# Performance work log

Hardware: AMD Instinct MI355X
Metric: run time of the kernel (lower is better)

## Reference

```python
import jax, jax.numpy as jnp
import numpy as np

B, L, D = 8, 2048, 256
NEG = 10000.0


def setup_inputs() -> dict:
    key = jax.random.key(0)
    kq, kk, kv, km = jax.random.split(key, 4)
    return {
        "query": jax.random.normal(kq, (B, L, D), dtype=jnp.float32),
        "key": jax.random.normal(kk, (B, L, D), dtype=jnp.float32),
        "value": jax.random.normal(kv, (B, L, D), dtype=jnp.float32),
        "mask": jax.random.randint(km, (B, L), 0, 2).astype(bool),
    }


def reference(query, key, value, mask):
    d = query.shape[-1]
    # scores: [B, Lq, Lk]
    e = jnp.einsum("bqd,bkd->bqk", query, key) / jnp.sqrt(jnp.asarray(d, query.dtype))
    # history_only (causal) mask: subtract 10000 where key index > query index
    q_len, k_len = query.shape[1], key.shape[1]
    causal = (jnp.arange(k_len)[None, :] > jnp.arange(q_len)[:, None]).astype(query.dtype)
    e = e - NEG * causal[None, :, :]
    # key padding mask: [B, 1, Lk]
    e = e - NEG * (1.0 - mask.astype(query.dtype))[:, None, :]
    attn = jax.nn.softmax(e, axis=-1)
    return jnp.einsum("bqk,bkd->bqd", attn, value)
```

## Files before the change

### kernel.cpp

```cpp
#include <hip/hip_runtime.h>
#include <stdint.h>

#define NL 2048
#define ND 256
#define KVB 32
#define QB 64
#define NQT 32
#define NT_ALL (NL / KVB)
#define CHUNK 10
#define NCHUNKS_B 125
#define TILE_BYTES (KVB * ND * 2)
#define IMG (8 * NT_ALL * TILE_BYTES)
#define WS_MB 256
#define WS_K (WS_MB + 2048)
#define WS_V (WS_K + IMG)
#define WS_P (WS_V + IMG)
#define PART_BYTES (QB * ND * 2 + QB * 8)

typedef __attribute__((ext_vector_type(8))) short short8;
typedef __attribute__((ext_vector_type(4))) short short4v;
typedef __attribute__((ext_vector_type(4))) float f32x4;
typedef __attribute__((ext_vector_type(4))) unsigned int u32x4;
typedef __attribute__((ext_vector_type(8))) unsigned short ushort8;

__device__ __forceinline__ unsigned short bf16rne(float x) {
  unsigned u = __builtin_bit_cast(unsigned, x);
  u += 0x7FFFu + ((u >> 16) & 1u);
  return (unsigned short)(u >> 16);
}

__device__ __forceinline__ short8 cvt8(float4 a, float4 b, float scale) {
  short8 v;
  v[0] = (short)bf16rne(a.x * scale);
  v[1] = (short)bf16rne(a.y * scale);
  v[2] = (short)bf16rne(a.z * scale);
  v[3] = (short)bf16rne(a.w * scale);
  v[4] = (short)bf16rne(b.x * scale);
  v[5] = (short)bf16rne(b.y * scale);
  v[6] = (short)bf16rne(b.z * scale);
  v[7] = (short)bf16rne(b.w * scale);
  return v;
}

__global__ __launch_bounds__(512)
void mask_pack(const unsigned* __restrict__ M, unsigned* __restrict__ MB) {
  __shared__ int badS;
  if (threadIdx.x == 0) badS = 0;
  __syncthreads();
  bool bad = false;
  for (int i = threadIdx.x; i < 4096; i += 512)
    if (M[i] > 1u) bad = true;
  if (__any(bad) && (threadIdx.x & 63) == 0) badS = 1;
  __syncthreads();
  const int byteMode = badS;
  const int i = threadIdx.x;
  unsigned m = 0;
  for (int j = 0; j < 32; ++j) {
    int mv = byteMode ? (int)((const unsigned char*)M)[i * 32 + j] : (int)M[i * 32 + j];
    m |= (mv ? 1u : 0u) << j;
  }
  MB[i] = m;
}

__global__ __launch_bounds__(128)
void convert_kv(const float* __restrict__ K, const float* __restrict__ V,
                unsigned char* __restrict__ ws) {
  const int t = blockIdx.x;
  const int b = t >> 6, tix = t & 63;
  const float* kt = K + ((size_t)b * NL + tix * KVB) * ND;
  const float* vt = V + ((size_t)b * NL + tix * KVB) * ND;
  unsigned char* kd = ws + WS_K + (size_t)t * TILE_BYTES;
  unsigned char* vd = ws + WS_V + (size_t)t * TILE_BYTES;
#pragma unroll
  for (int it = 0; it < 8; ++it) {
    int idx = it * 128 + threadIdx.x;
    int row = idx >> 5, u = idx & 31, f = u * 8;
    const float4* kp = (const float4*)(kt + (size_t)row * ND + f);
    int kb = (row * 512 + f * 2) ^ ((row & 7) << 4);
    *(short8*)(kd + kb) = cvt8(kp[0], kp[1], 1.0f);
    const float4* vp = (const float4*)(vt + (size_t)row * ND + f);
    int vb = (row >> 2) * 2048 + (u >> 1) * 128 + (row & 3) * 32 + (u & 1) * 16;
    *(short8*)(vd + vb) = cvt8(vp[0], vp[1], 1.0f);
  }
}

__global__ __launch_bounds__(256, 2)
void attn_fwd(const float* __restrict__ Qg, const unsigned* __restrict__ MBg,
              unsigned char* ws) {
  __shared__ unsigned short Ks[3][KVB * ND];
  __shared__ unsigned short Vs[2][KVB * ND];

  const int tid = threadIdx.x;
  const int wv = tid >> 6;
  const int lane = tid & 63;
  const int g = lane >> 4;
  const int cc = lane & 15;

  const int fid = blockIdx.x;
  const int b = fid / NCHUNKS_B;
  int rem = fid - b * NCHUNKS_B;
  int qt = 0, c = 0, pbase = 0;
  if (rem < 7) {
    qt = 0; c = rem; pbase = 0;
  } else {
    rem -= 7; pbase = 7;
    for (qt = 1; qt < NQT; ++qt) {
      int ncq = (2 * qt + 2 + CHUNK - 1) / CHUNK;
      if (rem < ncq) { c = rem; break; }
      rem -= ncq; pbase += ncq;
    }
  }
  const int qb = qt * QB;
  const int nt_s = (qt == 0) ? NT_ALL : (2 * qt + 2);
  const int t0 = c * CHUNK;
  const int t1 = min(nt_s, t0 + CHUNK);
  unsigned char* pp = ws + WS_P + (size_t)(b * NCHUNKS_B + pbase + c) * PART_BYTES;
  unsigned short* ppA = (unsigned short*)pp;
  float* ppM = (float*)(pp + QB * ND * 2);
  float* ppL = ppM + QB;

  auto stage_K = [&](int tix, int bi) {
    const unsigned char* kg = ws + WS_K + ((size_t)(b * NT_ALL + tix)) * TILE_BYTES;
#pragma unroll
    for (int s = 0; s < 4; ++s) {
      const int seg = wv * 4 + s;
      __builtin_amdgcn_global_load_lds(
          (const __attribute__((address_space(1))) unsigned int*)(kg + seg * 1024 + lane * 16),
          (__attribute__((address_space(3))) unsigned int*)((unsigned char*)&Ks[bi][0] + seg * 1024),
          16, 0, 0);
    }
  };
  auto stage_V = [&](int tix, int bi) {
    const unsigned char* vg = ws + WS_V + ((size_t)(b * NT_ALL + tix)) * TILE_BYTES;
#pragma unroll
    for (int s = 0; s < 4; ++s) {
      const int seg = wv * 4 + s;
      __builtin_amdgcn_global_load_lds(
          (const __attribute__((address_space(1))) unsigned int*)(vg + seg * 1024 + lane * 16),
          (__attribute__((address_space(3))) unsigned int*)((unsigned char*)&Vs[bi][0] + seg * 1024),
          16, 0, 0);
    }
  };

  const float* qp = Qg + ((size_t)b * NL + (qb + 16 * wv + cc)) * ND;
  short8 qf[8];
#pragma unroll
  for (int ch = 0; ch < 8; ++ch) {
    int f = ch * 32 + g * 8;
    float4 a0 = *reinterpret_cast<const float4*>(qp + f);
    float4 a1 = *reinterpret_cast<const float4*>(qp + f + 4);
    qf[ch] = cvt8(a0, a1, 0.0625f);
  }
  const int qg = qb + 16 * wv + cc;

  f32x4 acc[16];
#pragma unroll
  for (int i = 0; i < 16; ++i) acc[i] = (f32x4){0.f, 0.f, 0.f, 0.f};
  float m_run = -3.0e38f, l_run = 0.f;

  asm volatile("s_waitcnt vmcnt(0)" ::: "memory");
  __builtin_amdgcn_sched_barrier(0);
  stage_K(t0, t0 % 3);
  if (t0 + 1 < t1) stage_K(t0 + 1, (t0 + 1) % 3);
  stage_V(t0, t0 & 1);

  for (int tix = t0; tix < t1; ++tix) {
    if (tix + 2 < t1) stage_K(tix + 2, (tix + 2) % 3);
    if (tix + 1 < t1) stage_V(tix + 1, (tix + 1) & 1);
    if (tix + 2 < t1) {
      asm volatile("s_waitcnt vmcnt(8)" ::: "memory");
    } else if (tix + 1 < t1) {
      asm volatile("s_waitcnt vmcnt(4)" ::: "memory");
    } else {
      asm volatile("s_waitcnt vmcnt(0)" ::: "memory");
    }
    __builtin_amdgcn_sched_barrier(0);
    __builtin_amdgcn_s_barrier();
    __builtin_amdgcn_sched_barrier(0);

    const int kv0 = tix * KVB;
    const unsigned mb = MBg[b * NT_ALL + tix];

    const char* ksB = (const char*)&Ks[tix % 3][0];
    f32x4 s0 = {0.f, 0.f, 0.f, 0.f}, s1 = {0.f, 0.f, 0.f, 0.f};
    __builtin_amdgcn_s_setprio(1);
#pragma unroll
    for (int ch = 0; ch < 8; ++ch) {
      int cbase = ch * 64 + g * 16;
      int b0 = (cc * 512 + cbase) ^ ((cc & 7) << 4);
      int b1 = ((cc + 16) * 512 + cbase) ^ ((cc & 7) << 4);
      short8 k0 = *reinterpret_cast<const short8*>(ksB + b0);
      short8 k1 = *reinterpret_cast<const short8*>(ksB + b1);
      s0 = __builtin_amdgcn_mfma_f32_16x16x32_bf16(k0, qf[ch], s0, 0, 0, 0);
      s1 = __builtin_amdgcn_mfma_f32_16x16x32_bf16(k1, qf[ch], s1, 0, 0, 0);
    }
    __builtin_amdgcn_s_setprio(0);

#pragma unroll
    for (int r = 0; r < 4; ++r) {
      int k0i = 4 * g + r, k1i = 16 + 4 * g + r;
      if (!((mb >> k0i) & 1u)) s0[r] -= 10000.f;
      if (!((mb >> k1i) & 1u)) s1[r] -= 10000.f;
      if (kv0 + k0i > qg) s0[r] -= 10000.f;
      if (kv0 + k1i > qg) s1[r] -= 10000.f;
    }

    float rmax = fmaxf(fmaxf(fmaxf(s0[0], s0[1]), fmaxf(s0[2], s0[3])),
                       fmaxf(fmaxf(s1[0], s1[1]), fmaxf(s1[2], s1[3])));
    rmax = fmaxf(rmax, __shfl_xor(rmax, 16));
    rmax = fmaxf(rmax, __shfl_xor(rmax, 32));
    bool grow = (rmax > m_run + 8.f);
    if (__any(grow)) {
      float mn = fmaxf(m_run, rmax);
      float alpha = __expf(m_run - mn);
      m_run = mn;
      l_run *= alpha;
      f32x4 av;
#pragma unroll
      for (int r = 0; r < 4; ++r) av[r] = __shfl(alpha, 20 * g + r);
#pragma unroll
      for (int i = 0; i < 16; ++i) acc[i] *= av;
    }
    float p0[4], p1[4];
#pragma unroll
    for (int r = 0; r < 4; ++r) {
      p0[r] = __expf(s0[r] - m_run);
      p1[r] = __expf(s1[r] - m_run);
    }
    l_run += (p0[0] + p0[1]) + (p0[2] + p0[3]) +
             (p1[0] + p1[1]) + (p1[2] + p1[3]);

    unsigned a0, a1, b0w, b1w;
    asm("v_cvt_pk_bf16_f32 %0, %1, %2" : "=v"(a0) : "v"(p0[0]), "v"(p0[1]));
    asm("v_cvt_pk_bf16_f32 %0, %1, %2" : "=v"(a1) : "v"(p0[2]), "v"(p0[3]));
    asm("v_cvt_pk_bf16_f32 %0, %1, %2" : "=v"(b0w) : "v"(p1[0]), "v"(p1[1]));
    asm("v_cvt_pk_bf16_f32 %0, %1, %2" : "=v"(b1w) : "v"(p1[2]), "v"(p1[3]));
    const int srcLo = cc + ((g & 1) << 5);
    const int srcHi = srcLo + 16;
    unsigned wa0 = (unsigned)__shfl((int)a0, srcLo);
    unsigned wa1 = (unsigned)__shfl((int)a1, srcLo);
    unsigned wa2 = (unsigned)__shfl((int)a0, srcHi);
    unsigned wa3 = (unsigned)__shfl((int)a1, srcHi);
    unsigned wb0 = (unsigned)__shfl((int)b0w, srcLo);
    unsigned wb1 = (unsigned)__shfl((int)b1w, srcLo);
    unsigned wb2 = (unsigned)__shfl((int)b0w, srcHi);
    unsigned wb3 = (unsigned)__shfl((int)b1w, srcHi);
    const bool hiHalf = (g >= 2);
    u32x4 paw = {hiHalf ? wb0 : wa0, hiHalf ? wb1 : wa1,
                 hiHalf ? wb2 : wa2, hiHalf ? wb3 : wa3};
    short8 pa = __builtin_bit_cast(short8, paw);

    const unsigned va = (unsigned)(uintptr_t)&Vs[tix & 1][0] + g * 4096 + cc * 8;
    short4v lo[16], hi[16];
#pragma unroll
    for (int ft = 0; ft < 16; ++ft) {
      asm volatile("ds_read_b64_tr_b16 %0, %1 offset:%2"
                   : "=&v"(lo[ft]) : "v"(va), "i"(ft * 128) : "memory");
      asm volatile("ds_read_b64_tr_b16 %0, %1 offset:%2"
                   : "=&v"(hi[ft]) : "v"(va), "i"(ft * 128 + 2048) : "memory");
    }
    asm volatile("s_waitcnt lgkmcnt(15)" ::: "memory");
    __builtin_amdgcn_sched_barrier(0);
    __builtin_amdgcn_s_setprio(1);
#pragma unroll
    for (int ft = 0; ft < 8; ++ft) {
      short8 vb = __builtin_shufflevector(lo[ft], hi[ft], 0, 1, 2, 3, 4, 5, 6, 7);
      acc[ft] = __builtin_amdgcn_mfma_f32_16x16x32_bf16(pa, vb, acc[ft], 0, 0, 0);
    }
    __builtin_amdgcn_s_setprio(0);
    asm volatile("s_waitcnt lgkmcnt(0)" ::: "memory");
    __builtin_amdgcn_sched_barrier(0);
    __builtin_amdgcn_s_setprio(1);
#pragma unroll
    for (int ft = 8; ft < 16; ++ft) {
      short8 vb = __builtin_shufflevector(lo[ft], hi[ft], 0, 1, 2, 3, 4, 5, 6, 7);
      acc[ft] = __builtin_amdgcn_mfma_f32_16x16x32_bf16(pa, vb, acc[ft], 0, 0, 0);
    }
    __builtin_amdgcn_s_setprio(0);

    __builtin_amdgcn_sched_barrier(0);
    __builtin_amdgcn_s_barrier();
    __builtin_amdgcn_sched_barrier(0);
  }

  l_run += __shfl_xor(l_run, 16);
  l_run += __shfl_xor(l_run, 32);

  unsigned short* sc = &Ks[0][0];
#pragma unroll
  for (int ft = 0; ft < 16; ++ft) {
#pragma unroll
    for (int r = 0; r < 4; ++r) {
      sc[(16 * wv + 4 * g + r) * 256 + ft * 16 + cc] = bf16rne(acc[ft][r]);
    }
  }
  if (g == 0) {
    ppM[16 * wv + cc] = m_run;
    ppL[16 * wv + cc] = l_run;
  }
  __syncthreads();
  {
    const int row = tid >> 2, q4 = tid & 3;
    const unsigned short* srow = sc + row * 256 + q4 * 64;
#pragma unroll
    for (int kk = 0; kk < 8; ++kk) {
      *(ushort8*)(ppA + (size_t)row * ND + q4 * 64 + kk * 8) =
          *(const ushort8*)(srow + kk * 8);
    }
  }
}

__global__ __launch_bounds__(256)
void attn_combine(const unsigned char* __restrict__ ws, float* __restrict__ Og) {
  const int bid = blockIdx.x;
  const int b = bid >> 5, qt = bid & 31;
  const int tid = threadIdx.x;
  const int row = tid >> 2, sub = tid & 3;

  int pbase = 0, nc = 7;
  if (qt > 0) {
    pbase = 7;
    for (int j = 1; j < qt; ++j) pbase += (2 * j + 2 + CHUNK - 1) / CHUNK;
    nc = (2 * qt + 2 + CHUNK - 1) / CHUNK;
  }
  const unsigned char* p0 = ws + WS_P + (size_t)(b * NCHUNKS_B + pbase) * PART_BYTES;

  float M = -3.0e38f;
  for (int c = 0; c < nc; ++c) {
    M = fmaxf(M, *(const float*)(p0 + (size_t)c * PART_BYTES + QB * ND * 2 + row * 4));
  }
  float L = 0.f;
  float o[64];
#pragma unroll
  for (int j = 0; j < 64; ++j) o[j] = 0.f;
  for (int c = 0; c < nc; ++c) {
    const unsigned char* pc = p0 + (size_t)c * PART_BYTES;
    float mm = *(const float*)(pc + QB * ND * 2 + row * 4);
    float ll = *(const float*)(pc + QB * ND * 2 + QB * 4 + row * 4);
    float s = __expf(mm - M);
    L += ll * s;
    const unsigned short* pa =
        (const unsigned short*)pc + (size_t)row * ND + sub * 64;
#pragma unroll
    for (int kk = 0; kk < 8; ++kk) {
      ushort8 a = *(const ushort8*)(pa + kk * 8);
#pragma unroll
      for (int j = 0; j < 8; ++j) {
        unsigned u = ((unsigned)a[j]) << 16;
        o[kk * 8 + j] += __builtin_bit_cast(float, u) * s;
      }
    }
  }
  const float invL = 1.0f / L;
  float* op = Og + ((size_t)b * NL + qt * QB + row) * ND + sub * 64;
#pragma unroll
  for (int kk = 0; kk < 16; ++kk) {
    float4 v = {o[kk * 4] * invL, o[kk * 4 + 1] * invL, o[kk * 4 + 2] * invL,
                o[kk * 4 + 3] * invL};
    *(float4*)(op + kk * 4) = v;
  }
}

extern "C" void kernel_launch(void* const* d_in, const int* in_sizes, int n_in,
                              void* d_out, int out_size, void* d_ws, size_t ws_size,
                              hipStream_t stream) {
  (void)in_sizes; (void)n_in; (void)out_size; (void)ws_size;
  const float* Q = (const float*)d_in[0];
  const float* K = (const float*)d_in[1];
  const float* V = (const float*)d_in[2];
  const int* M = (const int*)d_in[3];
  unsigned char* ws = (unsigned char*)d_ws;

  mask_pack<<<dim3(1), dim3(512), 0, stream>>>((const unsigned*)M,
                                               (unsigned*)(ws + WS_MB));
  convert_kv<<<dim3(512), dim3(128), 0, stream>>>(K, V, ws);
  attn_fwd<<<dim3(8 * NCHUNKS_B), dim3(256), 0, stream>>>(
      Q, (const unsigned*)(ws + WS_MB), ws);
  attn_combine<<<dim3(256), dim3(256), 0, stream>>>(ws, (float*)d_out);
}
```

Baseline: 102.1 us.

## Double query tile to 128 rows with 8-wave blocks sharing K/V stages

After: 245.8 us. +140.8%, slower.

```diff
diff --git a/kernel.cpp b/kernel.cpp
--- a/kernel.cpp
+++ b/kernel.cpp
@@ -4,11 +4,11 @@
 #define NL 2048
 #define ND 256
 #define KVB 32
-#define QB 64
-#define NQT 32
+#define QB 128
+#define NPAIR 16
 #define NT_ALL (NL / KVB)
-#define CHUNK 10
-#define NCHUNKS_B 125
+#define CHUNK 12
+#define NCHUNKS_B 56
 #define TILE_BYTES (KVB * ND * 2)
 #define IMG (8 * NT_ALL * TILE_BYTES)
 #define WS_MB 256
@@ -84,7 +84,7 @@
   }
 }
 
-__global__ __launch_bounds__(256, 2)
+__global__ __launch_bounds__(512, 4)
 void attn_fwd(const float* __restrict__ Qg, const unsigned* __restrict__ MBg,
               unsigned char* ws) {
   __shared__ unsigned short Ks[3][KVB * ND];
@@ -99,19 +99,19 @@
   const int fid = blockIdx.x;
   const int b = fid / NCHUNKS_B;
   int rem = fid - b * NCHUNKS_B;
-  int qt = 0, c = 0, pbase = 0;
-  if (rem < 7) {
-    qt = 0; c = rem; pbase = 0;
+  int j = 0, c = 0, pbase = 0;
+  if (rem < 6) {
+    j = 0; c = rem; pbase = 0;
   } else {
-    rem -= 7; pbase = 7;
-    for (qt = 1; qt < NQT; ++qt) {
-      int ncq = (2 * qt + 2 + CHUNK - 1) / CHUNK;
+    rem -= 6; pbase = 6;
+    for (j = 1; j < NPAIR; ++j) {
+      int ncq = (4 * j + 4 + CHUNK - 1) / CHUNK;
       if (rem < ncq) { c = rem; break; }
       rem -= ncq; pbase += ncq;
     }
   }
-  const int qb = qt * QB;
-  const int nt_s = (qt == 0) ? NT_ALL : (2 * qt + 2);
+  const int qb = j * QB;
+  const int nt_s = (j == 0) ? NT_ALL : (4 * j + 4);
   const int t0 = c * CHUNK;
   const int t1 = min(nt_s, t0 + CHUNK);
   unsigned char* pp = ws + WS_P + (size_t)(b * NCHUNKS_B + pbase + c) * PART_BYTES;
@@ -122,8 +122,8 @@
   auto stage_K = [&](int tix, int bi) {
     const unsigned char* kg = ws + WS_K + ((size_t)(b * NT_ALL + tix)) * TILE_BYTES;
 #pragma unroll
-    for (int s = 0; s < 4; ++s) {
-      const int seg = wv * 4 + s;
+    for (int s = 0; s < 2; ++s) {
+      const int seg = wv * 2 + s;
       __builtin_amdgcn_global_load_lds(
           (const __attribute__((address_space(1))) unsigned int*)(kg + seg * 1024 + lane * 16),
           (__attribute__((address_space(3))) unsigned int*)((unsigned char*)&Ks[bi][0] + seg * 1024),
@@ -133,8 +133,8 @@
   auto stage_V = [&](int tix, int bi) {
     const unsigned char* vg = ws + WS_V + ((size_t)(b * NT_ALL + tix)) * TILE_BYTES;
 #pragma unroll
-    for (int s = 0; s < 4; ++s) {
-      const int seg = wv * 4 + s;
+    for (int s = 0; s < 2; ++s) {
+      const int seg = wv * 2 + s;
       __builtin_amdgcn_global_load_lds(
           (const __attribute__((address_space(1))) unsigned int*)(vg + seg * 1024 + lane * 16),
           (__attribute__((address_space(3))) unsigned int*)((unsigned char*)&Vs[bi][0] + seg * 1024),
@@ -161,14 +161,14 @@
   asm volatile("s_waitcnt vmcnt(0)" ::: "memory");
   __builtin_amdgcn_sched_barrier(0);
   stage_K(t0, t0 % 3);
+  stage_V(t0, t0 & 1);
   if (t0 + 1 < t1) stage_K(t0 + 1, (t0 + 1) % 3);
-  stage_V(t0, t0 & 1);
 
   for (int tix = t0; tix < t1; ++tix) {
+    if (tix + 1 < t1) stage_V(tix + 1, (tix + 1) & 1);
     if (tix + 2 < t1) stage_K(tix + 2, (tix + 2) % 3);
-    if (tix + 1 < t1) stage_V(tix + 1, (tix + 1) & 1);
     if (tix + 2 < t1) {
-      asm volatile("s_waitcnt vmcnt(8)" ::: "memory");
+      asm volatile("s_waitcnt vmcnt(6)" ::: "memory");
     } else if (tix + 1 < t1) {
       asm volatile("s_waitcnt vmcnt(4)" ::: "memory");
     } else {
@@ -285,74 +285,79 @@
 
   l_run += __shfl_xor(l_run, 16);
   l_run += __shfl_xor(l_run, 32);
-
-  unsigned short* sc = &Ks[0][0];
-#pragma unroll
-  for (int ft = 0; ft < 16; ++ft) {
-#pragma unroll
-    for (int r = 0; r < 4; ++r) {
-      sc[(16 * wv + 4 * g + r) * 256 + ft * 16 + cc] = bf16rne(acc[ft][r]);
-    }
-  }
   if (g == 0) {
     ppM[16 * wv + cc] = m_run;
     ppL[16 * wv + cc] = l_run;
   }
-  __syncthreads();
-  {
-    const int row = tid >> 2, q4 = tid & 3;
-    const unsigned short* srow = sc + row * 256 + q4 * 64;
-#pragma unroll
-    for (int kk = 0; kk < 8; ++kk) {
-      *(ushort8*)(ppA + (size_t)row * ND + q4 * 64 + kk * 8) =
-          *(const ushort8*)(srow + kk * 8);
-    }
+
+  unsigned short* sc = &Ks[0][0];
+#pragma unroll
+  for (int h = 0; h < 2; ++h) {
+    __syncthreads();
+    if ((wv >> 2) == h) {
+#pragma unroll
+      for (int ft = 0; ft < 16; ++ft) {
+#pragma unroll
+        for (int r = 0; r < 4; ++r) {
+          sc[(16 * (wv & 3) + 4 * g + r) * 256 + ft * 16 + cc] = bf16rne(acc[ft][r]);
+        }
+      }
+    }
+    __syncthreads();
+    const int row = tid >> 3, oct = tid & 7;
+    const ushort8* src = (const ushort8*)(sc + row * 256 + oct * 32);
+    ushort8* dst = (ushort8*)(ppA + (size_t)(h * 64 + row) * ND + oct * 32);
+#pragma unroll
+    for (int kk = 0; kk < 4; ++kk) dst[kk] = src[kk];
   }
 }
 
 __global__ __launch_bounds__(256)
 void attn_combine(const unsigned char* __restrict__ ws, float* __restrict__ Og) {
   const int bid = blockIdx.x;
-  const int b = bid >> 5, qt = bid & 31;
+  const int b = bid >> 5;
+  const int j = (bid >> 1) & 15;
+  const int h = bid & 1;
   const int tid = threadIdx.x;
   const int row = tid >> 2, sub = tid & 3;
-
-  int pbase = 0, nc = 7;
-  if (qt > 0) {
-    pbase = 7;
-    for (int j = 1; j < qt; ++j) pbase += (2 * j + 2 + CHUNK - 1) / CHUNK;
-    nc = (2 * qt + 2 + CHUNK - 1) / CHUNK;
+  const int grow = h * 64 + row;
+
+  int pbase = 0, nc = 6;
+  if (j > 0) {
+    pbase = 6;
+    for (int jj = 1; jj < j; ++jj) pbase += (4 * jj + 4 + CHUNK - 1) / CHUNK;
+    nc = (4 * j + 4 + CHUNK - 1) / CHUNK;
   }
   const unsigned char* p0 = ws + WS_P + (size_t)(b * NCHUNKS_B + pbase) * PART_BYTES;
 
   float M = -3.0e38f;
   for (int c = 0; c < nc; ++c) {
-    M = fmaxf(M, *(const float*)(p0 + (size_t)c * PART_BYTES + QB * ND * 2 + row * 4));
+    M = fmaxf(M, *(const float*)(p0 + (size_t)c * PART_BYTES + QB * ND * 2 + grow * 4));
   }
   float L = 0.f;
   float o[64];
 #pragma unroll
-  for (int j = 0; j < 64; ++j) o[j] = 0.f;
+  for (int q = 0; q < 64; ++q) o[q] = 0.f;
   for (int c = 0; c < nc; ++c) {
     const unsigned char* pc = p0 + (size_t)c * PART_BYTES;
-    float mm = *(const float*)(pc + QB * ND * 2 + row * 4);
-    float ll = *(const float*)(pc + QB * ND * 2 + QB * 4 + row * 4);
+    float mm = *(const float*)(pc + QB * ND * 2 + grow * 4);
+    float ll = *(const float*)(pc + QB * ND * 2 + QB * 4 + grow * 4);
     float s = __expf(mm - M);
     L += ll * s;
     const unsigned short* pa =
-        (const unsigned short*)pc + (size_t)row * ND + sub * 64;
+        (const unsigned short*)pc + (size_t)grow * ND + sub * 64;
 #pragma unroll
     for (int kk = 0; kk < 8; ++kk) {
       ushort8 a = *(const ushort8*)(pa + kk * 8);
 #pragma unroll
-      for (int j = 0; j < 8; ++j) {
-        unsigned u = ((unsigned)a[j]) << 16;
-        o[kk * 8 + j] += __builtin_bit_cast(float, u) * s;
+      for (int q = 0; q < 8; ++q) {
+        unsigned u = ((unsigned)a[q]) << 16;
+        o[kk * 8 + q] += __builtin_bit_cast(float, u) * s;
       }
     }
   }
   const float invL = 1.0f / L;
-  float* op = Og + ((size_t)b * NL + qt * QB + row) * ND + sub * 64;
+  float* op = Og + ((size_t)b * NL + j * QB + grow) * ND + sub * 64;
 #pragma unroll
   for (int kk = 0; kk < 16; ++kk) {
     float4 v = {o[kk * 4] * invL, o[kk * 4 + 1] * invL, o[kk * 4 + 2] * invL,
@@ -374,7 +379,7 @@
   mask_pack<<<dim3(1), dim3(512), 0, stream>>>((const unsigned*)M,
                                                (unsigned*)(ws + WS_MB));
   convert_kv<<<dim3(512), dim3(128), 0, stream>>>(K, V, ws);
-  attn_fwd<<<dim3(8 * NCHUNKS_B), dim3(256), 0, stream>>>(
+  attn_fwd<<<dim3(8 * NCHUNKS_B), dim3(512), 0, stream>>>(
       Q, (const unsigned*)(ws + WS_MB), ws);
   attn_combine<<<dim3(256), dim3(256), 0, stream>>>(ws, (float*)d_out);
 }
```
